# Kernel optimization log

Hardware: AMD Instinct MI355X
Metric: run time of the kernel (lower is better)

## Reference

```python
import jax, jax.numpy as jnp
import numpy as np

N, IN_DIM, HID, HEADS, LAYERS = 20000, 512, 128, 8, 2
E = 320000
C = HID // HEADS  # 16
NEG_SLOPE = 0.2   # PyG GATv2Conv default


def _layer_norm(h, g, b, eps=1e-5):
    mu = jnp.mean(h, axis=-1, keepdims=True)
    var = jnp.var(h, axis=-1, keepdims=True)
    return (h - mu) * jax.lax.rsqrt(var + eps) * g + b


def setup_inputs() -> dict:
    key = jax.random.key(0)
    ks = jax.random.split(key, 8)
    def glorot(k, shape, fan_in):
        return jax.random.normal(k, shape, jnp.float32) * np.float32(1.0 / np.sqrt(fan_in))
    x = jax.random.normal(ks[0], (N, IN_DIM), jnp.float32)
    edge_index = jax.random.randint(ks[1], (2, E), 0, N, dtype=jnp.int32)
    W_in = glorot(ks[2], (IN_DIM, HID), IN_DIM)
    b_in = jnp.zeros((HID,), jnp.float32)
    ln_in_g = jnp.ones((HID,), jnp.float32)
    ln_in_b = jnp.zeros((HID,), jnp.float32)
    Wl = glorot(ks[3], (LAYERS, HID, HID), HID)   # lin_l (source) per layer
    bl = jnp.zeros((LAYERS, HID), jnp.float32)
    Wr = glorot(ks[4], (LAYERS, HID, HID), HID)   # lin_r (target) per layer
    br = jnp.zeros((LAYERS, HID), jnp.float32)
    att = glorot(ks[5], (LAYERS, HEADS, C), C)    # attention vector a per head
    gat_bias = jnp.zeros((LAYERS, HID), jnp.float32)
    norm_g = jnp.ones((LAYERS, HID), jnp.float32)
    norm_b = jnp.zeros((LAYERS, HID), jnp.float32)
    return dict(x=x, edge_index=edge_index, W_in=W_in, b_in=b_in,
                ln_in_g=ln_in_g, ln_in_b=ln_in_b, Wl=Wl, bl=bl, Wr=Wr, br=br,
                att=att, gat_bias=gat_bias, norm_g=norm_g, norm_b=norm_b)


def reference(x, edge_index, W_in, b_in, ln_in_g, ln_in_b, Wl, bl, Wr, br, att, gat_bias, norm_g, norm_b):
    n = x.shape[0]
    # input_proj: Linear -> LayerNorm -> ReLU (dropout = identity at eval)
    h = jax.nn.relu(_layer_norm(x @ W_in + b_in, ln_in_g, ln_in_b))
    # add_self_loops=True
    loops = jnp.arange(n, dtype=edge_index.dtype)
    src = jnp.concatenate([edge_index[0], loops])
    dst = jnp.concatenate([edge_index[1], loops])
    for i in range(LAYERS):
        xl = (h @ Wl[i] + bl[i]).reshape(n, HEADS, C)  # transformed source feats
        xr = (h @ Wr[i] + br[i]).reshape(n, HEADS, C)  # transformed target feats
        # GATv2 score: a . LeakyReLU(xl[src] + xr[dst])  -> (E', H)
        e = jax.nn.leaky_relu(xl[src] + xr[dst], NEG_SLOPE)
        logits = jnp.einsum('ehc,hc->eh', e, att[i])
        # segment softmax over incoming edges of each dst node
        m = jax.ops.segment_max(logits, dst, num_segments=n)   # (N,H)
        ex = jnp.exp(logits - m[dst])
        s = jax.ops.segment_sum(ex, dst, num_segments=n)       # (N,H), >0 due to self loops
        alpha = ex / s[dst]
        # weighted scatter-add of source messages
        out = jax.ops.segment_sum(xl[src] * alpha[:, :, None], dst, num_segments=n)
        out = out.reshape(n, HID) + gat_bias[i]  # concat heads + bias
        # ELU -> (dropout=identity) -> residual -> LayerNorm
        h = _layer_norm(jax.nn.elu(out) + h, norm_g[i], norm_b[i])
    return h
```

## Files before the change

kernel.cpp:

```cpp
#include <hip/hip_runtime.h>
#include <math.h>

#define N_NODES 20000
#define IN_DIM  512
#define HID     128
#define HEADS   8
#define C_DIM   16
#define LAYERS  2
#define NEDGE   320000
#define NEG_SLOPE 0.2f
#define LN_EPS  1e-5f
#define CAP     64

#define PROJ_BLKS  625
#define EDGE_BLKS  ((NEDGE + 127) / 128)
#define SELF_BLKS  ((N_NODES + 127) / 128)

typedef __attribute__((ext_vector_type(8))) short short8;
typedef __attribute__((ext_vector_type(4))) float f32x4;

__device__ __forceinline__ unsigned short f2bf(float f) {
    unsigned int u = __float_as_uint(f);
    u += 0x7fffu + ((u >> 16) & 1u);
    return (unsigned short)(u >> 16);
}
__device__ __forceinline__ float bf2f(unsigned short s) {
    return __uint_as_float(((unsigned int)s) << 16);
}

__global__ __launch_bounds__(256) void k_convert(
    const float* __restrict__ W_in, const float* __restrict__ Wl, const float* __restrict__ Wr,
    unsigned short* __restrict__ WtI, unsigned short* __restrict__ Wlt, unsigned short* __restrict__ Wrt,
    int* __restrict__ cnt)
{
    int i = blockIdx.x * 256 + threadIdx.x;
    if (i < N_NODES) cnt[i] = 0;
    if (i < 65536) {
        int n = i & 127, k = i >> 7;
        WtI[(unsigned)n * IN_DIM + k] = f2bf(W_in[(unsigned)k * HID + n]);
    } else if (i < 98304) {
        int r = i - 65536;
        int L = r >> 14, q = r & 16383;
        int n = q & 127, k = q >> 7;
        Wlt[L * 16384 + n * HID + k] = f2bf(Wl[L * 16384 + k * HID + n]);
    } else if (i < 131072) {
        int r = i - 98304;
        int L = r >> 14, q = r & 16383;
        int n = q & 127, k = q >> 7;
        Wrt[L * 16384 + n * HID + k] = f2bf(Wr[L * 16384 + k * HID + n]);
    }
}

__global__ __launch_bounds__(128) void k_fused0(
    const float* __restrict__ x, const unsigned short* __restrict__ WtI,
    const float* __restrict__ b, const float* __restrict__ g, const float* __restrict__ beta,
    unsigned short* __restrict__ hb,
    const int* __restrict__ ei, int* __restrict__ cnt, int* __restrict__ adj)
{
    __shared__ unsigned short wlds[128][136];
    __shared__ unsigned short xtile[32][136];
    const int bid = blockIdx.x;
    const int tid = threadIdx.x;

    if (bid >= PROJ_BLKS) {
        if (bid < PROJ_BLKS + EDGE_BLKS) {
            int e = (bid - PROJ_BLKS) * 128 + tid;
            if (e < NEDGE) {
                int src = ei[e];
                int dst = ei[NEDGE + e];
                int r = atomicAdd(&cnt[dst], 1);
                if (r < CAP) adj[(unsigned)dst * CAP + r] = src;
            }
        } else {
            int i = (bid - PROJ_BLKS - EDGE_BLKS) * 128 + tid;
            if (i < N_NODES) {
                int r = atomicAdd(&cnt[i], 1);
                if (r < CAP) adj[(unsigned)i * CAP + r] = i;
            }
        }
        return;
    }

    const int wid = tid >> 6;
    const int l   = tid & 63;
    const int grp = l >> 4;
    const int ln  = l & 15;
    const int row0 = bid * 32;

    f32x4 acc[8];
#pragma unroll
    for (int j = 0; j < 8; ++j) acc[j] = (f32x4){0.f, 0.f, 0.f, 0.f};

    const int sr = tid >> 4;
    const int sc = (tid & 15) * 8;
    const int xrr = tid >> 2;
    const int xcc = (tid & 3) * 32;

    for (int kc = 0; kc < 4; ++kc) {
        __syncthreads();
#pragma unroll
        for (int rr = sr; rr < 128; rr += 8)
            *(short8*)&wlds[rr][sc] = *(const short8*)&WtI[rr * IN_DIM + kc * 128 + sc];
        {
            const float4* ps = (const float4*)&x[(unsigned)(row0 + xrr) * IN_DIM + kc * 128 + xcc];
#pragma unroll
            for (int q = 0; q < 4; ++q) {
                float4 va = ps[2 * q], vb = ps[2 * q + 1];
                short8 o;
                o[0] = (short)f2bf(va.x); o[1] = (short)f2bf(va.y);
                o[2] = (short)f2bf(va.z); o[3] = (short)f2bf(va.w);
                o[4] = (short)f2bf(vb.x); o[5] = (short)f2bf(vb.y);
                o[6] = (short)f2bf(vb.z); o[7] = (short)f2bf(vb.w);
                *(short8*)&xtile[xrr][xcc + q * 8] = o;
            }
        }
        __syncthreads();
#pragma unroll
        for (int ks = 0; ks < 4; ++ks) {
            short8 a = *(short8*)&xtile[wid * 16 + ln][ks * 32 + grp * 8];
#pragma unroll
            for (int j = 0; j < 8; ++j) {
                short8 bf = *(short8*)&wlds[j * 16 + ln][ks * 32 + grp * 8];
                acc[j] = __builtin_amdgcn_mfma_f32_16x16x32_bf16(a, bf, acc[j], 0, 0, 0);
            }
        }
    }
    float s1[4] = {0, 0, 0, 0}, s2[4] = {0, 0, 0, 0};
#pragma unroll
    for (int j = 0; j < 8; ++j) {
        float bb = b[j * 16 + ln];
#pragma unroll
        for (int r = 0; r < 4; ++r) {
            float v = acc[j][r] + bb;
            acc[j][r] = v;
            s1[r] += v; s2[r] += v * v;
        }
    }
#pragma unroll
    for (int r = 0; r < 4; ++r) {
#pragma unroll
        for (int off = 8; off; off >>= 1) {
            s1[r] += __shfl_xor(s1[r], off);
            s2[r] += __shfl_xor(s2[r], off);
        }
    }
#pragma unroll
    for (int r = 0; r < 4; ++r) {
        float mu  = s1[r] * (1.f / HID);
        float var = s2[r] * (1.f / HID) - mu * mu;
        float rs  = rsqrtf(var + LN_EPS);
        int row = row0 + wid * 16 + grp * 4 + r;
#pragma unroll
        for (int j = 0; j < 8; ++j) {
            int c = j * 16 + ln;
            float o = (acc[j][r] - mu) * rs * g[c] + beta[c];
            hb[(unsigned)row * HID + c] = f2bf(fmaxf(o, 0.f));
        }
    }
}

__global__ __launch_bounds__(128) void k_xlxr(
    const unsigned short* __restrict__ hb,
    const unsigned short* __restrict__ Wlt, const unsigned short* __restrict__ Wrt,
    const float* __restrict__ bl, const float* __restrict__ br,
    unsigned short* __restrict__ xlb, unsigned short* __restrict__ xrb)
{
    __shared__ unsigned short wl_lds[128][136];
    __shared__ unsigned short wr_lds[128][136];
    const int tid = threadIdx.x;
    const int wid = tid >> 6;
    const int l   = tid & 63;
    const int grp = l >> 4;
    const int ln  = l & 15;
    const int row0 = blockIdx.x * 32;
    const int arow = row0 + wid * 16 + ln;

    const int sr = tid >> 4;
    const int sc = (tid & 15) * 8;
#pragma unroll
    for (int rr = sr; rr < 128; rr += 8) {
        *(short8*)&wl_lds[rr][sc] = *(const short8*)&Wlt[rr * HID + sc];
        *(short8*)&wr_lds[rr][sc] = *(const short8*)&Wrt[rr * HID + sc];
    }
    __syncthreads();

    f32x4 aL[8], aR[8];
#pragma unroll
    for (int j = 0; j < 8; ++j) {
        aL[j] = (f32x4){0.f, 0.f, 0.f, 0.f};
        aR[j] = (f32x4){0.f, 0.f, 0.f, 0.f};
    }
#pragma unroll
    for (int ks = 0; ks < 4; ++ks) {
        const int kk = ks * 32 + grp * 8;
        short8 a = *(const short8*)&hb[(unsigned)arow * HID + kk];
#pragma unroll
        for (int j = 0; j < 8; ++j) {
            short8 b8l = *(short8*)&wl_lds[j * 16 + ln][kk];
            aL[j] = __builtin_amdgcn_mfma_f32_16x16x32_bf16(a, b8l, aL[j], 0, 0, 0);
            short8 b8r = *(short8*)&wr_lds[j * 16 + ln][kk];
            aR[j] = __builtin_amdgcn_mfma_f32_16x16x32_bf16(a, b8r, aR[j], 0, 0, 0);
        }
    }
#pragma unroll
    for (int r = 0; r < 4; ++r) {
        int row = row0 + wid * 16 + grp * 4 + r;
#pragma unroll
        for (int j = 0; j < 8; ++j) {
            int c = j * 16 + ln;
            xlb[(unsigned)row * HID + c] = f2bf(aL[j][r] + bl[c]);
            xrb[(unsigned)row * HID + c] = f2bf(aR[j][r] + br[c]);
        }
    }
}

#define PROC(xa, xb_, live) do {                                            \
    float xf[16];                                                           \
    _Pragma("unroll")                                                       \
    for (int q = 0; q < 8; ++q) {                                           \
        xf[q]     = bf2f((unsigned short)(xa)[q]);                          \
        xf[8 + q] = bf2f((unsigned short)(xb_)[q]);                         \
    }                                                                       \
    float ll = 0.f;                                                         \
    _Pragma("unroll")                                                       \
    for (int q = 0; q < 16; ++q) {                                          \
        float u = xf[q] + rv[q];                                            \
        u = fmaxf(u, NEG_SLOPE * u);                                        \
        ll = fmaf(av[q], u, ll);                                            \
    }                                                                       \
    float p = (live) ? __expf(ll) : 0.f;                                    \
    sp += p;                                                                \
    _Pragma("unroll")                                                       \
    for (int q = 0; q < 16; ++q) acc[q] = fmaf(p, xf[q], acc[q]);           \
} while (0)

__global__ __launch_bounds__(256) void k_gat(
    const unsigned short* __restrict__ xlb, const unsigned short* __restrict__ xrb,
    const int* __restrict__ adj, const int* __restrict__ cnt,
    const float* __restrict__ att, const float* __restrict__ gbias,
    const float* __restrict__ g, const float* __restrict__ beta,
    const unsigned short* __restrict__ hbin, float* __restrict__ hout,
    unsigned short* __restrict__ hbout)
{
    __shared__ float red[4][136];
    const int tid  = threadIdx.x;
    const int wv   = tid >> 6;
    const int lane = tid & 63;
    const int d    = blockIdx.x * 4 + wv;
    const int e    = lane >> 3;
    const int hh   = lane & 7;
    const int cb   = hh * 16;
    const unsigned dC = (unsigned)d * CAP;

    const int nj = min(cnt[d], CAP);
    int aj0 = adj[dC + e];
    int aj1 = adj[dC + 8 + e];
    int aj2 = adj[dC + 16 + e];

    float av[16], rv[16];
#pragma unroll
    for (int q = 0; q < 4; ++q) {
        float4 a4 = *(const float4*)&att[cb + q * 4];
        av[q*4+0] = a4.x; av[q*4+1] = a4.y; av[q*4+2] = a4.z; av[q*4+3] = a4.w;
    }
    {
        const short8* pr = (const short8*)&xrb[(unsigned)d * HID + cb];
        short8 r0 = pr[0], r1 = pr[1];
#pragma unroll
        for (int q = 0; q < 8; ++q) {
            rv[q]     = bf2f((unsigned short)r0[q]);
            rv[8 + q] = bf2f((unsigned short)r1[q]);
        }
    }

    const int src0 = (e < nj)      ? aj0 : d;
    const int src1 = (8 + e < nj)  ? aj1 : d;
    const int src2 = (16 + e < nj) ? aj2 : d;
    const short8* p0 = (const short8*)&xlb[(unsigned)src0 * HID + cb];
    short8 ga0 = p0[0], gb0 = p0[1];
    const short8* p1 = (const short8*)&xlb[(unsigned)src1 * HID + cb];
    short8 ga1 = p1[0], gb1 = p1[1];

    float acc[16];
#pragma unroll
    for (int q = 0; q < 16; ++q) acc[q] = 0.f;
    float sp = 0.f;

    if (nj > 16) {
        const short8* p2 = (const short8*)&xlb[(unsigned)src2 * HID + cb];
        short8 ga2 = p2[0], gb2 = p2[1];
        PROC(ga0, gb0, e < nj);
        PROC(ga1, gb1, true);
        PROC(ga2, gb2, 16 + e < nj);
        for (int ch = 3; (ch << 3) < nj; ++ch) {
            int j = (ch << 3) + e;
            int ajv = adj[dC + (j < nj ? j : 0)];
            int sj  = (j < nj) ? ajv : d;
            const short8* pj = (const short8*)&xlb[(unsigned)sj * HID + cb];
            short8 gaj = pj[0], gbj = pj[1];
            PROC(gaj, gbj, j < nj);
        }
    } else {
        PROC(ga0, gb0, e < nj);
        PROC(ga1, gb1, 8 + e < nj);
    }

#pragma unroll
    for (int m = 8; m < 64; m <<= 1) {
#pragma unroll
        for (int q = 0; q < 16; ++q) acc[q] += __shfl_xor(acc[q], m);
        sp += __shfl_xor(sp, m);
    }

    if (lane < 8) {
#pragma unroll
        for (int q = 0; q < 16; q += 4) {
            float4 v; v.x = acc[q]; v.y = acc[q+1]; v.z = acc[q+2]; v.w = acc[q+3];
            *(float4*)&red[wv][lane * 16 + q] = v;
        }
        red[wv][128 + lane] = sp;
    }
    const int c0 = lane * 2;
    float a0  = red[wv][c0];
    float a1  = red[wv][c0 + 1];
    float ssv = red[wv][128 + e];

    float2 gbv = *(const float2*)&gbias[c0];
    float2 ggv = *(const float2*)&g[c0];
    float2 bev = *(const float2*)&beta[c0];
    unsigned hr2 = *(const unsigned*)&hbin[(unsigned)d * HID + c0];

    float o0 = a0 / ssv + gbv.x;
    float o1 = a1 / ssv + gbv.y;
    o0 = o0 > 0.f ? o0 : (__expf(o0) - 1.f);
    o1 = o1 > 0.f ? o1 : (__expf(o1) - 1.f);
    o0 += bf2f((unsigned short)(hr2 & 0xffffu));
    o1 += bf2f((unsigned short)(hr2 >> 16));

    float s1l = o0 + o1, s2l = o0 * o0 + o1 * o1;
#pragma unroll
    for (int m = 1; m < 64; m <<= 1) {
        s1l += __shfl_xor(s1l, m);
        s2l += __shfl_xor(s2l, m);
    }
    float mu  = s1l * (1.f / HID);
    float var = s2l * (1.f / HID) - mu * mu;
    float rs  = rsqrtf(var + LN_EPS);
    float out0 = (o0 - mu) * rs * ggv.x + bev.x;
    float out1 = (o1 - mu) * rs * ggv.y + bev.y;
    if (hout) {
        float2 ov; ov.x = out0; ov.y = out1;
        *(float2*)&hout[(unsigned)d * HID + c0] = ov;
    }
    if (hbout) {
        unsigned pk = (unsigned)f2bf(out0) | ((unsigned)f2bf(out1) << 16);
        *(unsigned*)&hbout[(unsigned)d * HID + c0] = pk;
    }
}

extern "C" void kernel_launch(void* const* d_in, const int* in_sizes, int n_in,
                              void* d_out, int out_size, void* d_ws, size_t ws_size,
                              hipStream_t stream) {
    (void)in_sizes; (void)n_in; (void)out_size; (void)ws_size;
    const float* x        = (const float*)d_in[0];
    const int*   ei       = (const int*)  d_in[1];
    const float* W_in     = (const float*)d_in[2];
    const float* b_in     = (const float*)d_in[3];
    const float* ln_g     = (const float*)d_in[4];
    const float* ln_b     = (const float*)d_in[5];
    const float* Wl       = (const float*)d_in[6];
    const float* bl       = (const float*)d_in[7];
    const float* Wr       = (const float*)d_in[8];
    const float* br       = (const float*)d_in[9];
    const float* att      = (const float*)d_in[10];
    const float* gat_bias = (const float*)d_in[11];
    const float* norm_g   = (const float*)d_in[12];
    const float* norm_b   = (const float*)d_in[13];
    float* out_f = (float*)d_out;

    char* w = (char*)d_ws;
    int*   adj = (int*)w;                           w += (size_t)N_NODES * CAP * 4;
    int*   cnt = (int*)w;                           w += (size_t)N_NODES * 4;
    unsigned short* hb  = (unsigned short*)w;       w += (size_t)N_NODES * HID * 2;
    unsigned short* xlb = (unsigned short*)w;       w += (size_t)N_NODES * HID * 2;
    unsigned short* xrb = (unsigned short*)w;       w += (size_t)N_NODES * HID * 2;
    unsigned short* WtI = (unsigned short*)w;       w += (size_t)IN_DIM * HID * 2;
    unsigned short* Wlt = (unsigned short*)w;       w += (size_t)LAYERS * HID * HID * 2;
    unsigned short* Wrt = (unsigned short*)w;

    k_convert<<<512, 256, 0, stream>>>(W_in, Wl, Wr, WtI, Wlt, Wrt, cnt);
    k_fused0<<<PROJ_BLKS + EDGE_BLKS + SELF_BLKS, 128, 0, stream>>>(
        x, WtI, b_in, ln_g, ln_b, hb, ei, cnt, adj);

    for (int L = 0; L < LAYERS; ++L) {
        k_xlxr<<<N_NODES / 32, 128, 0, stream>>>(
            hb, Wlt + (size_t)L * HID * HID, Wrt + (size_t)L * HID * HID,
            bl + (size_t)L * HID, br + (size_t)L * HID, xlb, xrb);
        float*          hout   = (L == LAYERS - 1) ? out_f : (float*)nullptr;
        unsigned short* hbnext = (L == LAYERS - 1) ? (unsigned short*)nullptr : hb;
        k_gat<<<N_NODES / 4, 256, 0, stream>>>(
            xlb, xrb, adj, cnt,
            att + (size_t)L * HEADS * C_DIM, gat_bias + (size_t)L * HID,
            norm_g + (size_t)L * HID, norm_b + (size_t)L * HID, hb, hout, hbnext);
    }
}
```

Measured before the change: 123.5 us.

## Split input projection across four waves by output columns with 16-row tiles

The input projection kernel now uses 256-thread blocks over 16-row tiles, and each of the four waves computes a 32-column slice instead of each wave owning 16 rows across all 128 columns. LayerNorm statistics are combined across waves through a small shared-memory reduction and an extra barrier. Edge and self-loop blocks are resized to 256 threads to match. The aim is more blocks and more waves in flight to hide the memory-bound x loads, at the cost of reloading the full weight tile per 16 rows, which doubles weight LDS traffic per output row.

Measured after the change: 124.3 us. Within noise of the previous version (+0.7%).

```diff
diff --git a/kernel.cpp b/kernel.cpp
--- a/kernel.cpp
+++ b/kernel.cpp
@@ -12,9 +12,9 @@
 #define LN_EPS  1e-5f
 #define CAP     64
 
-#define PROJ_BLKS  625
-#define EDGE_BLKS  ((NEDGE + 127) / 128)
-#define SELF_BLKS  ((N_NODES + 127) / 128)
+#define PROJ_BLKS  1250
+#define EDGE_BLKS  ((NEDGE + 255) / 256)
+#define SELF_BLKS  ((N_NODES + 255) / 256)
 
 typedef __attribute__((ext_vector_type(8))) short short8;
 typedef __attribute__((ext_vector_type(4))) float f32x4;
@@ -51,20 +51,21 @@
     }
 }
 
-__global__ __launch_bounds__(128) void k_fused0(
+__global__ __launch_bounds__(256) void k_fused0(
     const float* __restrict__ x, const unsigned short* __restrict__ WtI,
     const float* __restrict__ b, const float* __restrict__ g, const float* __restrict__ beta,
     unsigned short* __restrict__ hb,
     const int* __restrict__ ei, int* __restrict__ cnt, int* __restrict__ adj)
 {
     __shared__ unsigned short wlds[128][136];
-    __shared__ unsigned short xtile[32][136];
+    __shared__ unsigned short xtile[16][136];
+    __shared__ float redm[4][16][2];
     const int bid = blockIdx.x;
     const int tid = threadIdx.x;
 
     if (bid >= PROJ_BLKS) {
         if (bid < PROJ_BLKS + EDGE_BLKS) {
-            int e = (bid - PROJ_BLKS) * 128 + tid;
+            int e = (bid - PROJ_BLKS) * 256 + tid;
             if (e < NEDGE) {
                 int src = ei[e];
                 int dst = ei[NEDGE + e];
@@ -72,7 +73,7 @@
                 if (r < CAP) adj[(unsigned)dst * CAP + r] = src;
             }
         } else {
-            int i = (bid - PROJ_BLKS - EDGE_BLKS) * 128 + tid;
+            int i = (bid - PROJ_BLKS - EDGE_BLKS) * 256 + tid;
             if (i < N_NODES) {
                 int r = atomicAdd(&cnt[i], 1);
                 if (r < CAP) adj[(unsigned)i * CAP + r] = i;
@@ -81,54 +82,52 @@
         return;
     }
 
-    const int wid = tid >> 6;
+    const int wv  = tid >> 6;
     const int l   = tid & 63;
     const int grp = l >> 4;
     const int ln  = l & 15;
-    const int row0 = bid * 32;
-
-    f32x4 acc[8];
-#pragma unroll
-    for (int j = 0; j < 8; ++j) acc[j] = (f32x4){0.f, 0.f, 0.f, 0.f};
-
-    const int sr = tid >> 4;
-    const int sc = (tid & 15) * 8;
-    const int xrr = tid >> 2;
-    const int xcc = (tid & 3) * 32;
+    const int row0 = bid * 16;
+
+    f32x4 acc[2];
+    acc[0] = (f32x4){0.f, 0.f, 0.f, 0.f};
+    acc[1] = (f32x4){0.f, 0.f, 0.f, 0.f};
+
+    const int sr  = tid >> 4;
+    const int sc  = (tid & 15) * 8;
+    const int xrr = tid >> 4;
+    const int xcc = (tid & 15) * 8;
 
     for (int kc = 0; kc < 4; ++kc) {
         __syncthreads();
 #pragma unroll
-        for (int rr = sr; rr < 128; rr += 8)
+        for (int rr = sr; rr < 128; rr += 16)
             *(short8*)&wlds[rr][sc] = *(const short8*)&WtI[rr * IN_DIM + kc * 128 + sc];
         {
             const float4* ps = (const float4*)&x[(unsigned)(row0 + xrr) * IN_DIM + kc * 128 + xcc];
-#pragma unroll
-            for (int q = 0; q < 4; ++q) {
-                float4 va = ps[2 * q], vb = ps[2 * q + 1];
-                short8 o;
-                o[0] = (short)f2bf(va.x); o[1] = (short)f2bf(va.y);
-                o[2] = (short)f2bf(va.z); o[3] = (short)f2bf(va.w);
-                o[4] = (short)f2bf(vb.x); o[5] = (short)f2bf(vb.y);
-                o[6] = (short)f2bf(vb.z); o[7] = (short)f2bf(vb.w);
-                *(short8*)&xtile[xrr][xcc + q * 8] = o;
-            }
+            float4 va = ps[0], vb = ps[1];
+            short8 o;
+            o[0] = (short)f2bf(va.x); o[1] = (short)f2bf(va.y);
+            o[2] = (short)f2bf(va.z); o[3] = (short)f2bf(va.w);
+            o[4] = (short)f2bf(vb.x); o[5] = (short)f2bf(vb.y);
+            o[6] = (short)f2bf(vb.z); o[7] = (short)f2bf(vb.w);
+            *(short8*)&xtile[xrr][xcc] = o;
         }
         __syncthreads();
 #pragma unroll
         for (int ks = 0; ks < 4; ++ks) {
-            short8 a = *(short8*)&xtile[wid * 16 + ln][ks * 32 + grp * 8];
-#pragma unroll
-            for (int j = 0; j < 8; ++j) {
-                short8 bf = *(short8*)&wlds[j * 16 + ln][ks * 32 + grp * 8];
+            short8 a = *(short8*)&xtile[ln][ks * 32 + grp * 8];
+#pragma unroll
+            for (int j = 0; j < 2; ++j) {
+                short8 bf = *(short8*)&wlds[wv * 32 + j * 16 + ln][ks * 32 + grp * 8];
                 acc[j] = __builtin_amdgcn_mfma_f32_16x16x32_bf16(a, bf, acc[j], 0, 0, 0);
             }
         }
     }
+
     float s1[4] = {0, 0, 0, 0}, s2[4] = {0, 0, 0, 0};
 #pragma unroll
-    for (int j = 0; j < 8; ++j) {
-        float bb = b[j * 16 + ln];
+    for (int j = 0; j < 2; ++j) {
+        float bb = b[wv * 32 + j * 16 + ln];
 #pragma unroll
         for (int r = 0; r < 4; ++r) {
             float v = acc[j][r] + bb;
@@ -144,17 +143,27 @@
             s2[r] += __shfl_xor(s2[r], off);
         }
     }
+    if (ln == 0) {
+#pragma unroll
+        for (int r = 0; r < 4; ++r) {
+            redm[wv][grp * 4 + r][0] = s1[r];
+            redm[wv][grp * 4 + r][1] = s2[r];
+        }
+    }
+    __syncthreads();
 #pragma unroll
     for (int r = 0; r < 4; ++r) {
-        float mu  = s1[r] * (1.f / HID);
-        float var = s2[r] * (1.f / HID) - mu * mu;
+        int row = grp * 4 + r;
+        float S1 = redm[0][row][0] + redm[1][row][0] + redm[2][row][0] + redm[3][row][0];
+        float S2 = redm[0][row][1] + redm[1][row][1] + redm[2][row][1] + redm[3][row][1];
+        float mu  = S1 * (1.f / HID);
+        float var = S2 * (1.f / HID) - mu * mu;
         float rs  = rsqrtf(var + LN_EPS);
-        int row = row0 + wid * 16 + grp * 4 + r;
-#pragma unroll
-        for (int j = 0; j < 8; ++j) {
-            int c = j * 16 + ln;
+#pragma unroll
+        for (int j = 0; j < 2; ++j) {
+            int c = wv * 32 + j * 16 + ln;
             float o = (acc[j][r] - mu) * rs * g[c] + beta[c];
-            hb[(unsigned)row * HID + c] = f2bf(fmaxf(o, 0.f));
+            hb[(unsigned)(row0 + row) * HID + c] = f2bf(fmaxf(o, 0.f));
         }
     }
 }
@@ -389,7 +398,7 @@
     unsigned short* Wrt = (unsigned short*)w;
 
     k_convert<<<512, 256, 0, stream>>>(W_in, Wl, Wr, WtI, Wlt, Wrt, cnt);
-    k_fused0<<<PROJ_BLKS + EDGE_BLKS + SELF_BLKS, 128, 0, stream>>>(
+    k_fused0<<<PROJ_BLKS + EDGE_BLKS + SELF_BLKS, 256, 0, stream>>>(
         x, WtI, b_in, ln_g, ln_b, hb, ei, cnt, adj);
 
     for (int L = 0; L < LAYERS; ++L) {
```

## Split input projection into bf16 pre-swizzle pass and LDS-free MFMA GEMM

Applied to the files above, without the earlier changes.

The fused input-projection kernel is split in two. A prep kernel converts x to bf16 in an MFMA-fragment-ordered layout while also building the adjacency lists. A separate projection kernel then loads A fragments straight from global memory and streams weights from global without LDS staging or barriers. Edge counters are padded to one per 64 bytes to reduce atomic contention on shared cache lines. This adds an extra 20 MB bf16 round trip and an extra launch, and weights are now re-read from global/L2 per wave instead of shared through LDS.

Result: slower. 151.6 us (+22.8%).

```diff
diff --git a/kernel.cpp b/kernel.cpp
--- a/kernel.cpp
+++ b/kernel.cpp
@@ -12,9 +12,9 @@
 #define LN_EPS  1e-5f
 #define CAP     64
 
-#define PROJ_BLKS  625
-#define EDGE_BLKS  ((NEDGE + 127) / 128)
-#define SELF_BLKS  ((N_NODES + 127) / 128)
+#define XB_BLKS    1250
+#define EDGE_BLKS  ((NEDGE + 255) / 256)
+#define SELF_BLKS  ((N_NODES + 255) / 256)
 
 typedef __attribute__((ext_vector_type(8))) short short8;
 typedef __attribute__((ext_vector_type(4))) float f32x4;
@@ -28,13 +28,13 @@
     return __uint_as_float(((unsigned int)s) << 16);
 }
 
-__global__ __launch_bounds__(256) void k_convert(
+__global__ __launch_bounds__(256) void k_wconv(
     const float* __restrict__ W_in, const float* __restrict__ Wl, const float* __restrict__ Wr,
     unsigned short* __restrict__ WtI, unsigned short* __restrict__ Wlt, unsigned short* __restrict__ Wrt,
-    int* __restrict__ cnt)
+    int* __restrict__ cntp)
 {
     int i = blockIdx.x * 256 + threadIdx.x;
-    if (i < N_NODES) cnt[i] = 0;
+    if (i < N_NODES) cntp[i << 4] = 0;
     if (i < 65536) {
         int n = i & 127, k = i >> 7;
         WtI[(unsigned)n * IN_DIM + k] = f2bf(W_in[(unsigned)k * HID + n]);
@@ -51,80 +51,94 @@
     }
 }
 
-__global__ __launch_bounds__(128) void k_fused0(
-    const float* __restrict__ x, const unsigned short* __restrict__ WtI,
-    const float* __restrict__ b, const float* __restrict__ g, const float* __restrict__ beta,
-    unsigned short* __restrict__ hb,
-    const int* __restrict__ ei, int* __restrict__ cnt, int* __restrict__ adj)
+__global__ __launch_bounds__(256) void k_prep(
+    const float* __restrict__ x, unsigned short* __restrict__ xbB,
+    const int* __restrict__ ei, int* __restrict__ cntp, int* __restrict__ adj)
 {
-    __shared__ unsigned short wlds[128][136];
-    __shared__ unsigned short xtile[32][136];
+    __shared__ unsigned short xl[16][520];
     const int bid = blockIdx.x;
-    const int tid = threadIdx.x;
-
-    if (bid >= PROJ_BLKS) {
-        if (bid < PROJ_BLKS + EDGE_BLKS) {
-            int e = (bid - PROJ_BLKS) * 128 + tid;
+    const int t   = threadIdx.x;
+
+    if (bid >= XB_BLKS) {
+        if (bid < XB_BLKS + EDGE_BLKS) {
+            int e = (bid - XB_BLKS) * 256 + t;
             if (e < NEDGE) {
                 int src = ei[e];
                 int dst = ei[NEDGE + e];
-                int r = atomicAdd(&cnt[dst], 1);
+                int r = atomicAdd(&cntp[dst << 4], 1);
                 if (r < CAP) adj[(unsigned)dst * CAP + r] = src;
             }
         } else {
-            int i = (bid - PROJ_BLKS - EDGE_BLKS) * 128 + tid;
+            int i = (bid - XB_BLKS - EDGE_BLKS) * 256 + t;
             if (i < N_NODES) {
-                int r = atomicAdd(&cnt[i], 1);
+                int r = atomicAdd(&cntp[i << 4], 1);
                 if (r < CAP) adj[(unsigned)i * CAP + r] = i;
             }
         }
         return;
     }
 
+    {
+        const int row  = t >> 4;
+        const int col0 = (t & 15) * 32;
+        const float4* ps = (const float4*)&x[(unsigned)(bid * 16 + row) * IN_DIM + col0];
+#pragma unroll
+        for (int q = 0; q < 4; ++q) {
+            float4 va = ps[2 * q], vb = ps[2 * q + 1];
+            short8 o;
+            o[0] = (short)f2bf(va.x); o[1] = (short)f2bf(va.y);
+            o[2] = (short)f2bf(va.z); o[3] = (short)f2bf(va.w);
+            o[4] = (short)f2bf(vb.x); o[5] = (short)f2bf(vb.y);
+            o[6] = (short)f2bf(vb.z); o[7] = (short)f2bf(vb.w);
+            *(short8*)&xl[row][col0 + q * 8] = o;
+        }
+    }
+    __syncthreads();
+
+    unsigned short* outb = &xbB[(unsigned)bid * 8192];
+#pragma unroll
+    for (int i = 0; i < 4; ++i) {
+        int g   = i * 256 + t;
+        int row = g & 15;
+        int grp = (g >> 4) & 3;
+        int ks  = g >> 6;
+        short8 v = *(short8*)&xl[row][ks * 32 + grp * 8];
+        *(short8*)&outb[ks * 512 + grp * 128 + row * 8] = v;
+    }
+}
+
+__global__ __launch_bounds__(128) void k_proj(
+    const unsigned short* __restrict__ xbB, const unsigned short* __restrict__ WtI,
+    const float* __restrict__ b, const float* __restrict__ g, const float* __restrict__ beta,
+    unsigned short* __restrict__ hb)
+{
+    const int tid = threadIdx.x;
     const int wid = tid >> 6;
     const int l   = tid & 63;
     const int grp = l >> 4;
     const int ln  = l & 15;
-    const int row0 = bid * 32;
+    const int R    = blockIdx.x * 2 + wid;
+    const int row0 = R * 16;
+
+    short8 a[16];
+    const unsigned short* pa = &xbB[(unsigned)R * 8192 + grp * 128 + ln * 8];
+#pragma unroll
+    for (int ks = 0; ks < 16; ++ks)
+        a[ks] = *(const short8*)&pa[ks * 512];
 
     f32x4 acc[8];
 #pragma unroll
     for (int j = 0; j < 8; ++j) acc[j] = (f32x4){0.f, 0.f, 0.f, 0.f};
-
-    const int sr = tid >> 4;
-    const int sc = (tid & 15) * 8;
-    const int xrr = tid >> 2;
-    const int xcc = (tid & 3) * 32;
-
-    for (int kc = 0; kc < 4; ++kc) {
-        __syncthreads();
-#pragma unroll
-        for (int rr = sr; rr < 128; rr += 8)
-            *(short8*)&wlds[rr][sc] = *(const short8*)&WtI[rr * IN_DIM + kc * 128 + sc];
-        {
-            const float4* ps = (const float4*)&x[(unsigned)(row0 + xrr) * IN_DIM + kc * 128 + xcc];
-#pragma unroll
-            for (int q = 0; q < 4; ++q) {
-                float4 va = ps[2 * q], vb = ps[2 * q + 1];
-                short8 o;
-                o[0] = (short)f2bf(va.x); o[1] = (short)f2bf(va.y);
-                o[2] = (short)f2bf(va.z); o[3] = (short)f2bf(va.w);
-                o[4] = (short)f2bf(vb.x); o[5] = (short)f2bf(vb.y);
-                o[6] = (short)f2bf(vb.z); o[7] = (short)f2bf(vb.w);
-                *(short8*)&xtile[xrr][xcc + q * 8] = o;
-            }
-        }
-        __syncthreads();
-#pragma unroll
-        for (int ks = 0; ks < 4; ++ks) {
-            short8 a = *(short8*)&xtile[wid * 16 + ln][ks * 32 + grp * 8];
-#pragma unroll
-            for (int j = 0; j < 8; ++j) {
-                short8 bf = *(short8*)&wlds[j * 16 + ln][ks * 32 + grp * 8];
-                acc[j] = __builtin_amdgcn_mfma_f32_16x16x32_bf16(a, bf, acc[j], 0, 0, 0);
-            }
-        }
-    }
+#pragma unroll
+    for (int j = 0; j < 8; ++j) {
+        const unsigned short* pw = &WtI[(unsigned)(j * 16 + ln) * IN_DIM + grp * 8];
+#pragma unroll
+        for (int ks = 0; ks < 16; ++ks) {
+            short8 bf = *(const short8*)&pw[ks * 32];
+            acc[j] = __builtin_amdgcn_mfma_f32_16x16x32_bf16(a[ks], bf, acc[j], 0, 0, 0);
+        }
+    }
+
     float s1[4] = {0, 0, 0, 0}, s2[4] = {0, 0, 0, 0};
 #pragma unroll
     for (int j = 0; j < 8; ++j) {
@@ -149,7 +163,7 @@
         float mu  = s1[r] * (1.f / HID);
         float var = s2[r] * (1.f / HID) - mu * mu;
         float rs  = rsqrtf(var + LN_EPS);
-        int row = row0 + wid * 16 + grp * 4 + r;
+        int row = row0 + grp * 4 + r;
 #pragma unroll
         for (int j = 0; j < 8; ++j) {
             int c = j * 16 + ln;
@@ -236,7 +250,7 @@
 
 __global__ __launch_bounds__(256) void k_gat(
     const unsigned short* __restrict__ xlb, const unsigned short* __restrict__ xrb,
-    const int* __restrict__ adj, const int* __restrict__ cnt,
+    const int* __restrict__ adj, const int* __restrict__ cntp,
     const float* __restrict__ att, const float* __restrict__ gbias,
     const float* __restrict__ g, const float* __restrict__ beta,
     const unsigned short* __restrict__ hbin, float* __restrict__ hout,
@@ -252,7 +266,7 @@
     const int cb   = hh * 16;
     const unsigned dC = (unsigned)d * CAP;
 
-    const int nj = min(cnt[d], CAP);
+    const int nj = min(cntp[d << 4], CAP);
     int aj0 = adj[dC + e];
     int aj1 = adj[dC + 8 + e];
     int aj2 = adj[dC + 16 + e];
@@ -379,8 +393,9 @@
     float* out_f = (float*)d_out;
 
     char* w = (char*)d_ws;
-    int*   adj = (int*)w;                           w += (size_t)N_NODES * CAP * 4;
-    int*   cnt = (int*)w;                           w += (size_t)N_NODES * 4;
+    int*   adj  = (int*)w;                          w += (size_t)N_NODES * CAP * 4;
+    int*   cntp = (int*)w;                          w += (size_t)N_NODES * 64;
+    unsigned short* xbB = (unsigned short*)w;       w += (size_t)N_NODES * IN_DIM * 2;
     unsigned short* hb  = (unsigned short*)w;       w += (size_t)N_NODES * HID * 2;
     unsigned short* xlb = (unsigned short*)w;       w += (size_t)N_NODES * HID * 2;
     unsigned short* xrb = (unsigned short*)w;       w += (size_t)N_NODES * HID * 2;
@@ -388,9 +403,9 @@
     unsigned short* Wlt = (unsigned short*)w;       w += (size_t)LAYERS * HID * HID * 2;
     unsigned short* Wrt = (unsigned short*)w;
 
-    k_convert<<<512, 256, 0, stream>>>(W_in, Wl, Wr, WtI, Wlt, Wrt, cnt);
-    k_fused0<<<PROJ_BLKS + EDGE_BLKS + SELF_BLKS, 128, 0, stream>>>(
-        x, WtI, b_in, ln_g, ln_b, hb, ei, cnt, adj);
+    k_wconv<<<512, 256, 0, stream>>>(W_in, Wl, Wr, WtI, Wlt, Wrt, cntp);
+    k_prep<<<XB_BLKS + EDGE_BLKS + SELF_BLKS, 256, 0, stream>>>(x, xbB, ei, cntp, adj);
+    k_proj<<<N_NODES / 32, 128, 0, stream>>>(xbB, WtI, b_in, ln_g, ln_b, hb);
 
     for (int L = 0; L < LAYERS; ++L) {
         k_xlxr<<<N_NODES / 32, 128, 0, stream>>>(
@@ -399,7 +414,7 @@
         float*          hout   = (L == LAYERS - 1) ? out_f : (float*)nullptr;
         unsigned short* hbnext = (L == LAYERS - 1) ? (unsigned short*)nullptr : hb;
         k_gat<<<N_NODES / 4, 256, 0, stream>>>(
-            xlb, xrb, adj, cnt,
+            xlb, xrb, adj, cntp,
             att + (size_t)L * HEADS * C_DIM, gat_bias + (size_t)L * HID,
             norm_g + (size_t)L * HID, norm_b + (size_t)L * HID, hb, hout, hbnext);
     }
```
